# Kernel optimization log

Measured on AMD Instinct MI355X. Metric: run time of the kernel, lower is better.

## Reference

```python
import jax, jax.numpy as jnp
import numpy as np

NUM_CLASSES = 20
NUM_ANC = 5
S_ = 1 + NUM_CLASSES                   # 21
GDIM = 1 + NUM_CLASSES + 4 + 1 + 4     # 30: conf, cls20, txywh4, weight, gltrb4
ANCS_SCALE = np.array([[0.05, 0.07], [0.12, 0.15], [0.25, 0.30], [0.45, 0.55], [0.75, 0.80]], dtype=np.float32)
LOSS_W_CLS = 1.0
EPS16 = 0.0009765625  # torch.finfo(torch.float16).eps
BATCH, GRID, NBOX = 64, 38, 16
C_IN = (S_ + 4) * NUM_ANC              # 125


def ltrb2xywh(b):
    return jnp.concatenate([(b[..., :2] + b[..., 2:]) * 0.5, b[..., 2:] - b[..., :2]], -1)


def x_bce(p, g):
    p = jnp.clip(p, EPS16, 1.0 - EPS16)
    return -(g * jnp.log(p) + (1.0 - g) * jnp.log(1.0 - p))


def match_one(gboxes, glabels, ancs, grid):
    # gboxes [N,4] ltrb in [0,1]; glabels [N] in [1,NUM_CLASSES]
    xywh = ltrb2xywh(gboxes)
    cxy, wh = xywh[:, :2], xywh[:, 2:]
    # IoU between co-centered GT wh and anchor wh (both centered at origin)
    inter = jnp.minimum(wh[:, None, 0], ancs[None, :, 0]) * jnp.minimum(wh[:, None, 1], ancs[None, :, 1])
    union = (wh[:, 0] * wh[:, 1])[:, None] + (ancs[:, 0] * ancs[:, 1])[None, :] - inter
    ids_p = jnp.argmax(inter / union, axis=-1)                           # [N] best anchor per GT
    colrow = jnp.clip(jnp.floor(cxy * grid).astype(jnp.int32), 0, grid - 1)
    txy = cxy * grid - colrow.astype(cxy.dtype)                          # cell-relative offset
    twh = jnp.log(wh / ancs[ids_p])                                      # log wh ratio vs matched anchor
    weight = 2.0 - wh[:, 0] * wh[:, 1]
    onehot = jax.nn.one_hot(glabels - 1, NUM_CLASSES, dtype=gboxes.dtype)
    ones = jnp.ones((gboxes.shape[0], 1), gboxes.dtype)
    tvec = jnp.concatenate([ones, onehot, txy, twh, weight[:, None], gboxes], -1)  # [N,GDIM]
    g = jnp.zeros((grid, grid, NUM_ANC, GDIM), gboxes.dtype)
    col, row = colrow[:, 0], colrow[:, 1]
    g = g.at[row, col, :, 0].set(-1.0)       # mark all anchors at GT cell as ignore
    g = g.at[row, col, ids_p].set(tvec)      # matched anchor gets full target (conf=1)
    return g


def _loss(pyolos, gboxes_ltrb, glabels):
    batch, c, h, w = pyolos.shape
    p = pyolos.reshape(batch, S_ + 4, NUM_ANC, h * w)
    p = p.transpose(0, 3, 2, 1).reshape(batch, -1, S_ + 4)               # [B, h*w*A, 25]
    ancs = jnp.asarray(ANCS_SCALE)
    gy = jax.vmap(lambda b, l: match_one(b, l, ancs, h))(gboxes_ltrb, glabels)
    gy = gy.reshape(batch, -1, GDIM)                                     # [B, h*w*A, 30]
    gconf = gy[:, :, 0]
    mask_pos = gconf > 0
    mask_neg = gconf == 0
    nums_pos = jnp.clip(mask_pos.sum(-1).astype(jnp.float32), EPS16)
    nums_neg = jnp.clip(mask_neg.sum(-1).astype(jnp.float32), EPS16)
    mpf = mask_pos.astype(p.dtype)
    n_pos_tot = jnp.maximum(mpf.sum(), 1.0)
    # ---- cls loss over positives (masked mean == .mean() over selected) ----
    pcls = jax.nn.sigmoid(p[:, :, 1:S_])
    l_cls = (x_bce(pcls, gy[:, :, 1:S_]).sum(-1) * mpf).sum() / n_pos_tot * LOSS_W_CLS
    # ---- conf focal loss (alpha=0.5, gamma=2), replicating sum(-1).sum(-1)/nums then mean ----
    pconf = jnp.clip(jax.nn.sigmoid(p[:, :, 0]), EPS16, 1.0 - EPS16)
    l_pos = -0.5 * (1.0 - pconf) ** 2 * jnp.log(pconf) * gconf * mpf
    l_neg = -0.5 * pconf ** 2 * jnp.log(1.0 - pconf) * (1.0 - gconf) * mask_neg.astype(p.dtype)
    l_conf_pos = (l_pos.sum() / nums_pos).mean()
    l_conf_neg = (l_neg.sum() / nums_neg).mean() * 3.0
    # ---- box loss (MODE_TRAIN != 4 branch). NB: original indexes weight at S_+4+1 ----
    pxy = jax.nn.sigmoid(p[:, :, S_:S_ + 2])
    pwh = p[:, :, S_ + 2:S_ + 4]
    w_pos = gy[:, :, S_ + 4 + 1]
    l_txty = ((x_bce(pxy, gy[:, :, S_:S_ + 2]).sum(-1) * w_pos) * mpf).sum() / n_pos_tot
    l_twth = ((((pwh - gy[:, :, S_ + 2:S_ + 4]) ** 2).sum(-1) * w_pos) * mpf).sum() / n_pos_tot
    return l_conf_pos + l_conf_neg + l_cls + l_txty + l_twth


def setup_inputs():
    key = jax.random.key(0)
    k1, k2, k3, k4 = jax.random.split(key, 4)
    pyolos = jax.random.normal(k1, (BATCH, C_IN, GRID, GRID), jnp.float32)
    cxy = jax.random.uniform(k2, (BATCH, NBOX, 2), jnp.float32, 0.1, 0.9)
    wh = jax.random.uniform(k3, (BATCH, NBOX, 2), jnp.float32, 0.05, 0.3)
    gboxes_ltrb = jnp.concatenate([cxy - wh * 0.5, cxy + wh * 0.5], -1)
    glabels = jax.random.randint(k4, (BATCH, NBOX), 1, NUM_CLASSES + 1)
    return {"pyolos": pyolos, "gboxes_ltrb": gboxes_ltrb, "glabels": glabels}


def reference(pyolos, gboxes_ltrb, glabels):
    return _loss(pyolos, gboxes_ltrb, glabels)
```

## Files before the change

### kernel.cpp

```cpp
#include <hip/hip_runtime.h>

#define BATCH 64
#define GRIDW 38
#define HW 1444
#define NBOX 16
#define NANC 5
#define NCLS 20
#define SLOTS 7220
#define CIN 125
#define EPSC 0.0009765625f
#define BPB 29
#define NBLK (BATCH * BPB)

struct BoxRec {
  int   cell;
  int   ids;
  int   lab;
  float tx, ty, tw, th;
  float wleft;
};

__constant__ float ANCW[5] = {0.05f, 0.12f, 0.25f, 0.45f, 0.75f};
__constant__ float ANCH[5] = {0.07f, 0.15f, 0.30f, 0.55f, 0.80f};

__global__ void match_kernel(const float* __restrict__ gboxes,
                             const int* __restrict__ glabels,
                             BoxRec* __restrict__ recs) {
  int b = threadIdx.x;
  if (b >= BATCH) return;
  const float* gb = gboxes + (size_t)b * NBOX * 4;
  const int*   gl = glabels + (size_t)b * NBOX;
  for (int n = 0; n < NBOX; ++n) {
    float l  = gb[n * 4 + 0], t = gb[n * 4 + 1];
    float r  = gb[n * 4 + 2], bt = gb[n * 4 + 3];
    float cx = (l + r) * 0.5f, cy = (t + bt) * 0.5f;
    float w  = r - l,          h  = bt - t;
    int best = 0; float bestv = -1.0f;
    for (int a = 0; a < NANC; ++a) {
      float inter = fminf(w, ANCW[a]) * fminf(h, ANCH[a]);
      float uni   = w * h + ANCW[a] * ANCH[a] - inter;
      float iou   = inter / uni;
      if (iou > bestv) { bestv = iou; best = a; }
    }
    int col = (int)floorf(cx * (float)GRIDW);
    int row = (int)floorf(cy * (float)GRIDW);
    col = min(max(col, 0), GRIDW - 1);
    row = min(max(row, 0), GRIDW - 1);
    BoxRec rec;
    rec.cell  = row * GRIDW + col;
    rec.ids   = best;
    rec.lab   = gl[n] - 1;
    rec.tx    = cx * (float)GRIDW - (float)col;
    rec.ty    = cy * (float)GRIDW - (float)row;
    rec.tw    = logf(w / ANCW[best]);
    rec.th    = logf(h / ANCH[best]);
    rec.wleft = l;
    recs[b * NBOX + n] = rec;
  }
}

__global__ void __launch_bounds__(256) main_kernel(
    const float* __restrict__ pyolos,
    const BoxRec* __restrict__ recs,
    float* __restrict__ partials,
    int* __restrict__ pos_cnt,
    int* __restrict__ ign_cnt) {
  int b     = blockIdx.x / BPB;
  int chunk = blockIdx.x - b * BPB;

  __shared__ BoxRec sbox[NBOX];
  if (threadIdx.x < NBOX * 8) {
    ((int*)sbox)[threadIdx.x] = ((const int*)(recs + (size_t)b * NBOX))[threadIdx.x];
  }
  __syncthreads();

  float s_pos = 0.f, s_neg = 0.f, s_cls = 0.f, s_txty = 0.f, s_twth = 0.f;
  int c_pos = 0, c_ign = 0;

  int sIdx = chunk * 256 + threadIdx.x;
  if (sIdx < SLOTS) {
    int j = sIdx / HW;
    int k = sIdx - j * HW;

    int posbox = -1; bool cellmatch = false;
    #pragma unroll
    for (int n = 0; n < NBOX; ++n) {
      if (sbox[n].cell == k) {
        cellmatch = true;
        if (sbox[n].ids == j) posbox = n;
      }
    }

    const float* pb = pyolos + (size_t)b * CIN * HW + k;
    float pconf = 1.0f / (1.0f + expf(-pb[(size_t)j * HW]));
    pconf = fminf(fmaxf(pconf, EPSC), 1.0f - EPSC);

    if (posbox >= 0) {
      c_pos = 1;
      float om = 1.0f - pconf;
      s_pos = -0.5f * om * om * logf(pconf);
      BoxRec rec = sbox[posbox];
      float csum = 0.f;
      for (int c = 0; c < NCLS; ++c) {
        float pc = 1.0f / (1.0f + expf(-pb[(size_t)((1 + c) * NANC + j) * HW]));
        pc = fminf(fmaxf(pc, EPSC), 1.0f - EPSC);
        csum += (c == rec.lab) ? -logf(pc) : -logf(1.0f - pc);
      }
      s_cls = csum;
      float px = 1.0f / (1.0f + expf(-pb[(size_t)(21 * NANC + j) * HW]));
      float py = 1.0f / (1.0f + expf(-pb[(size_t)(22 * NANC + j) * HW]));
      px = fminf(fmaxf(px, EPSC), 1.0f - EPSC);
      py = fminf(fmaxf(py, EPSC), 1.0f - EPSC);
      float bx = -(rec.tx * logf(px) + (1.0f - rec.tx) * logf(1.0f - px));
      float by = -(rec.ty * logf(py) + (1.0f - rec.ty) * logf(1.0f - py));
      s_txty = (bx + by) * rec.wleft;
      float pw = pb[(size_t)(23 * NANC + j) * HW];
      float ph = pb[(size_t)(24 * NANC + j) * HW];
      float dw = pw - rec.tw, dh = ph - rec.th;
      s_twth = (dw * dw + dh * dh) * rec.wleft;
    } else if (cellmatch) {
      c_ign = 1;
    } else {
      s_neg = -0.5f * pconf * pconf * logf(1.0f - pconf);
    }
  }

  __shared__ float red[4][5];
  __shared__ int   redi[4][2];
  int lane = threadIdx.x & 63;
  int wid  = threadIdx.x >> 6;
  for (int off = 32; off; off >>= 1) {
    s_pos  += __shfl_down(s_pos,  off, 64);
    s_neg  += __shfl_down(s_neg,  off, 64);
    s_cls  += __shfl_down(s_cls,  off, 64);
    s_txty += __shfl_down(s_txty, off, 64);
    s_twth += __shfl_down(s_twth, off, 64);
    c_pos  += __shfl_down(c_pos,  off, 64);
    c_ign  += __shfl_down(c_ign,  off, 64);
  }
  if (lane == 0) {
    red[wid][0] = s_pos;  red[wid][1] = s_neg; red[wid][2] = s_cls;
    red[wid][3] = s_txty; red[wid][4] = s_twth;
    redi[wid][0] = c_pos; redi[wid][1] = c_ign;
  }
  __syncthreads();
  if (threadIdx.x == 0) {
    float a0 = 0, a1 = 0, a2 = 0, a3 = 0, a4 = 0; int p = 0, g = 0;
    for (int w2 = 0; w2 < 4; ++w2) {
      a0 += red[w2][0]; a1 += red[w2][1]; a2 += red[w2][2];
      a3 += red[w2][3]; a4 += red[w2][4];
      p += redi[w2][0]; g += redi[w2][1];
    }
    float* mine = partials + (size_t)blockIdx.x * 5;
    mine[0] = a0; mine[1] = a1; mine[2] = a2; mine[3] = a3; mine[4] = a4;
    if (p) atomicAdd(&pos_cnt[b], p);
    if (g) atomicAdd(&ign_cnt[b], g);
  }
}

__global__ void finalize_kernel(const float* __restrict__ partials,
                                const int* __restrict__ pos_cnt,
                                const int* __restrict__ ign_cnt,
                                float* __restrict__ out) {
  double a[5] = {0, 0, 0, 0, 0};
  for (int i = threadIdx.x; i < NBLK; i += 256) {
    const float* p = partials + (size_t)i * 5;
    a[0] += p[0]; a[1] += p[1]; a[2] += p[2]; a[3] += p[3]; a[4] += p[4];
  }
  __shared__ double redd[4][5];
  int lane = threadIdx.x & 63;
  int wid  = threadIdx.x >> 6;
  for (int off = 32; off; off >>= 1)
    for (int q = 0; q < 5; ++q) a[q] += __shfl_down(a[q], off, 64);
  if (lane == 0)
    for (int q = 0; q < 5; ++q) redd[wid][q] = a[q];

  double inv_pos = 0, inv_neg = 0, npos = 0;
  if (threadIdx.x < BATCH) {
    double posf = (double)pos_cnt[threadIdx.x];
    double negf = (double)(SLOTS - pos_cnt[threadIdx.x] - ign_cnt[threadIdx.x]);
    inv_pos = 1.0 / fmax(posf, (double)EPSC);
    inv_neg = 1.0 / fmax(negf, (double)EPSC);
    npos = posf;
  }
  for (int off = 32; off; off >>= 1) {
    inv_pos += __shfl_down(inv_pos, off, 64);
    inv_neg += __shfl_down(inv_neg, off, 64);
    npos    += __shfl_down(npos,    off, 64);
  }
  __syncthreads();
  if (threadIdx.x == 0) {
    double s[5] = {0, 0, 0, 0, 0};
    for (int w2 = 0; w2 < 4; ++w2)
      for (int q = 0; q < 5; ++q) s[q] += redd[w2][q];
    double n_pos_tot = fmax(npos, 1.0);
    double loss = s[0] * (inv_pos / (double)BATCH)
                + 3.0 * s[1] * (inv_neg / (double)BATCH)
                + s[2] / n_pos_tot
                + s[3] / n_pos_tot
                + s[4] / n_pos_tot;
    out[0] = (float)loss;
  }
}

extern "C" void kernel_launch(void* const* d_in, const int* in_sizes, int n_in,
                              void* d_out, int out_size, void* d_ws, size_t ws_size,
                              hipStream_t stream) {
  const float* pyolos  = (const float*)d_in[0];
  const float* gboxes  = (const float*)d_in[1];
  const int*   glabels = (const int*)d_in[2];
  float* out = (float*)d_out;

  char* base = (char*)d_ws;
  BoxRec* recs     = (BoxRec*)base;
  float*  partials = (float*)(base + 32768);
  int*    pos_cnt  = (int*)(base + 69888);
  int*    ign_cnt  = (int*)(base + 70144);

  hipMemsetAsync(base + 69888, 0, 512, stream);
  match_kernel<<<1, 64, 0, stream>>>(gboxes, glabels, recs);
  main_kernel<<<NBLK, 256, 0, stream>>>(pyolos, recs, partials, pos_cnt, ign_cnt);
  finalize_kernel<<<1, 256, 0, stream>>>(partials, pos_cnt, ign_cnt, out);
}
```

Baseline: 111.0 us.

## Fuse GT matching into main kernel and drop memset and atomics

Every block of the main kernel now does the per-image box matching itself, using 16 threads to fill shared memory, so the separate single-block match kernel goes away. The per-image positive and ignore counts are stored as floats in the per-block partials, and the finalize kernel sums them there. This removes the memset, the global atomics and one kernel launch, leaving two launches instead of four operations. The cost is redundant matching work in each of the 29 blocks per image and float counters instead of integer ones.

Measured after the change: 96.75 us, median of 2. 1.15x faster.

```diff
diff --git a/kernel.cpp b/kernel.cpp
--- a/kernel.cpp
+++ b/kernel.cpp
@@ -11,6 +11,7 @@
 #define EPSC 0.0009765625f
 #define BPB 29
 #define NBLK (BATCH * BPB)
+#define PSTRIDE 7
 
 struct BoxRec {
   int   cell;
@@ -23,19 +24,23 @@
 __constant__ float ANCW[5] = {0.05f, 0.12f, 0.25f, 0.45f, 0.75f};
 __constant__ float ANCH[5] = {0.07f, 0.15f, 0.30f, 0.55f, 0.80f};
 
-__global__ void match_kernel(const float* __restrict__ gboxes,
-                             const int* __restrict__ glabels,
-                             BoxRec* __restrict__ recs) {
-  int b = threadIdx.x;
-  if (b >= BATCH) return;
-  const float* gb = gboxes + (size_t)b * NBOX * 4;
-  const int*   gl = glabels + (size_t)b * NBOX;
-  for (int n = 0; n < NBOX; ++n) {
-    float l  = gb[n * 4 + 0], t = gb[n * 4 + 1];
-    float r  = gb[n * 4 + 2], bt = gb[n * 4 + 3];
+__global__ void __launch_bounds__(256) main_kernel(
+    const float* __restrict__ pyolos,
+    const float* __restrict__ gboxes,
+    const int* __restrict__ glabels,
+    float* __restrict__ partials) {
+  int b     = blockIdx.x / BPB;
+  int chunk = blockIdx.x - b * BPB;
+
+  __shared__ BoxRec sbox[NBOX];
+  if (threadIdx.x < NBOX) {
+    int n = threadIdx.x;
+    const float* gb = gboxes + ((size_t)b * NBOX + n) * 4;
+    float l  = gb[0], t = gb[1], r = gb[2], bt = gb[3];
     float cx = (l + r) * 0.5f, cy = (t + bt) * 0.5f;
     float w  = r - l,          h  = bt - t;
     int best = 0; float bestv = -1.0f;
+    #pragma unroll
     for (int a = 0; a < NANC; ++a) {
       float inter = fminf(w, ANCW[a]) * fminf(h, ANCH[a]);
       float uni   = w * h + ANCW[a] * ANCH[a] - inter;
@@ -49,33 +54,18 @@
     BoxRec rec;
     rec.cell  = row * GRIDW + col;
     rec.ids   = best;
-    rec.lab   = gl[n] - 1;
+    rec.lab   = glabels[(size_t)b * NBOX + n] - 1;
     rec.tx    = cx * (float)GRIDW - (float)col;
     rec.ty    = cy * (float)GRIDW - (float)row;
     rec.tw    = logf(w / ANCW[best]);
     rec.th    = logf(h / ANCH[best]);
     rec.wleft = l;
-    recs[b * NBOX + n] = rec;
-  }
-}
-
-__global__ void __launch_bounds__(256) main_kernel(
-    const float* __restrict__ pyolos,
-    const BoxRec* __restrict__ recs,
-    float* __restrict__ partials,
-    int* __restrict__ pos_cnt,
-    int* __restrict__ ign_cnt) {
-  int b     = blockIdx.x / BPB;
-  int chunk = blockIdx.x - b * BPB;
-
-  __shared__ BoxRec sbox[NBOX];
-  if (threadIdx.x < NBOX * 8) {
-    ((int*)sbox)[threadIdx.x] = ((const int*)(recs + (size_t)b * NBOX))[threadIdx.x];
+    sbox[n] = rec;
   }
   __syncthreads();
 
   float s_pos = 0.f, s_neg = 0.f, s_cls = 0.f, s_txty = 0.f, s_twth = 0.f;
-  int c_pos = 0, c_ign = 0;
+  float c_pos = 0.f, c_ign = 0.f;
 
   int sIdx = chunk * 256 + threadIdx.x;
   if (sIdx < SLOTS) {
@@ -96,7 +86,7 @@
     pconf = fminf(fmaxf(pconf, EPSC), 1.0f - EPSC);
 
     if (posbox >= 0) {
-      c_pos = 1;
+      c_pos = 1.f;
       float om = 1.0f - pconf;
       s_pos = -0.5f * om * om * logf(pconf);
       BoxRec rec = sbox[posbox];
@@ -119,14 +109,13 @@
       float dw = pw - rec.tw, dh = ph - rec.th;
       s_twth = (dw * dw + dh * dh) * rec.wleft;
     } else if (cellmatch) {
-      c_ign = 1;
+      c_ign = 1.f;
     } else {
       s_neg = -0.5f * pconf * pconf * logf(1.0f - pconf);
     }
   }
 
-  __shared__ float red[4][5];
-  __shared__ int   redi[4][2];
+  __shared__ float red[4][PSTRIDE];
   int lane = threadIdx.x & 63;
   int wid  = threadIdx.x >> 6;
   for (int off = 32; off; off >>= 1) {
@@ -141,30 +130,23 @@
   if (lane == 0) {
     red[wid][0] = s_pos;  red[wid][1] = s_neg; red[wid][2] = s_cls;
     red[wid][3] = s_txty; red[wid][4] = s_twth;
-    redi[wid][0] = c_pos; redi[wid][1] = c_ign;
+    red[wid][5] = c_pos;  red[wid][6] = c_ign;
   }
   __syncthreads();
   if (threadIdx.x == 0) {
-    float a0 = 0, a1 = 0, a2 = 0, a3 = 0, a4 = 0; int p = 0, g = 0;
-    for (int w2 = 0; w2 < 4; ++w2) {
-      a0 += red[w2][0]; a1 += red[w2][1]; a2 += red[w2][2];
-      a3 += red[w2][3]; a4 += red[w2][4];
-      p += redi[w2][0]; g += redi[w2][1];
-    }
-    float* mine = partials + (size_t)blockIdx.x * 5;
-    mine[0] = a0; mine[1] = a1; mine[2] = a2; mine[3] = a3; mine[4] = a4;
-    if (p) atomicAdd(&pos_cnt[b], p);
-    if (g) atomicAdd(&ign_cnt[b], g);
+    float a[PSTRIDE] = {0, 0, 0, 0, 0, 0, 0};
+    for (int w2 = 0; w2 < 4; ++w2)
+      for (int q = 0; q < PSTRIDE; ++q) a[q] += red[w2][q];
+    float* mine = partials + (size_t)blockIdx.x * PSTRIDE;
+    for (int q = 0; q < PSTRIDE; ++q) mine[q] = a[q];
   }
 }
 
 __global__ void finalize_kernel(const float* __restrict__ partials,
-                                const int* __restrict__ pos_cnt,
-                                const int* __restrict__ ign_cnt,
                                 float* __restrict__ out) {
   double a[5] = {0, 0, 0, 0, 0};
   for (int i = threadIdx.x; i < NBLK; i += 256) {
-    const float* p = partials + (size_t)i * 5;
+    const float* p = partials + (size_t)i * PSTRIDE;
     a[0] += p[0]; a[1] += p[1]; a[2] += p[2]; a[3] += p[3]; a[4] += p[4];
   }
   __shared__ double redd[4][5];
@@ -177,8 +159,11 @@
 
   double inv_pos = 0, inv_neg = 0, npos = 0;
   if (threadIdx.x < BATCH) {
-    double posf = (double)pos_cnt[threadIdx.x];
-    double negf = (double)(SLOTS - pos_cnt[threadIdx.x] - ign_cnt[threadIdx.x]);
+    float p = 0.f, g = 0.f;
+    const float* pp = partials + (size_t)threadIdx.x * BPB * PSTRIDE;
+    for (int i = 0; i < BPB; ++i) { p += pp[i * PSTRIDE + 5]; g += pp[i * PSTRIDE + 6]; }
+    double posf = (double)p;
+    double negf = (double)SLOTS - (double)p - (double)g;
     inv_pos = 1.0 / fmax(posf, (double)EPSC);
     inv_neg = 1.0 / fmax(negf, (double)EPSC);
     npos = posf;
@@ -211,14 +196,8 @@
   const int*   glabels = (const int*)d_in[2];
   float* out = (float*)d_out;
 
-  char* base = (char*)d_ws;
-  BoxRec* recs     = (BoxRec*)base;
-  float*  partials = (float*)(base + 32768);
-  int*    pos_cnt  = (int*)(base + 69888);
-  int*    ign_cnt  = (int*)(base + 70144);
-
-  hipMemsetAsync(base + 69888, 0, 512, stream);
-  match_kernel<<<1, 64, 0, stream>>>(gboxes, glabels, recs);
-  main_kernel<<<NBLK, 256, 0, stream>>>(pyolos, recs, partials, pos_cnt, ign_cnt);
-  finalize_kernel<<<1, 256, 0, stream>>>(partials, pos_cnt, ign_cnt, out);
+  float* partials = (float*)d_ws;
+
+  main_kernel<<<NBLK, 256, 0, stream>>>(pyolos, gboxes, glabels, partials);
+  finalize_kernel<<<1, 256, 0, stream>>>(partials, out);
 }
```
